# Kernel optimization log

Measured on AMD Instinct MI355X. Metric: run time of the kernel, lower is better.

Reference implementation:

```python
import jax, jax.numpy as jnp
import numpy as np

D_MODEL = 1024
N_HEADS = 16
HEAD_DIM = D_MODEL // N_HEADS
SPARSITY = 0.5  # torch.rand(...) < sparsity_factor -> True means masked (disallowed)


def setup_inputs() -> dict:
    key = jax.random.key(0)
    ks = jax.random.split(key, 12)
    B, S, D = 2, 2048, D_MODEL
    query = jax.random.normal(ks[0], (B, S, D), dtype=jnp.float32)
    key_t = jax.random.normal(ks[1], (B, S, D), dtype=jnp.float32)
    value = jax.random.normal(ks[2], (B, S, D), dtype=jnp.float32)
    # per-forward random boolean mask, materialized deterministically here
    mask = jax.random.uniform(ks[3], (B, S, S)) < SPARSITY
    scale = 1.0 / np.sqrt(D)
    Wq = jax.random.uniform(ks[4], (D, D), jnp.float32, -scale, scale)
    Wk = jax.random.uniform(ks[5], (D, D), jnp.float32, -scale, scale)
    Wv = jax.random.uniform(ks[6], (D, D), jnp.float32, -scale, scale)
    Wo = jax.random.uniform(ks[7], (D, D), jnp.float32, -scale, scale)
    bq = jnp.zeros((D,), jnp.float32)
    bk = jnp.zeros((D,), jnp.float32)
    bv = jnp.zeros((D,), jnp.float32)
    bo = jnp.zeros((D,), jnp.float32)
    return {"query": query, "key": key_t, "value": value, "mask": mask,
            "Wq": Wq, "Wk": Wk, "Wv": Wv, "Wo": Wo,
            "bq": bq, "bk": bk, "bv": bv, "bo": bo}


def reference(query, key, value, mask, Wq, Wk, Wv, Wo, bq, bk, bv, bo):
    B, S, D = query.shape
    H, hd = N_HEADS, HEAD_DIM
    # in-projections (torch uses x @ W.T + b)
    q = (query @ Wq.T + bq).reshape(B, S, H, hd).transpose(0, 2, 1, 3)  # (B,H,S,hd)
    k = (key @ Wk.T + bk).reshape(B, S, H, hd).transpose(0, 2, 1, 3)
    v = (value @ Wv.T + bv).reshape(B, S, H, hd).transpose(0, 2, 1, 3)
    scores = jnp.einsum('bhqd,bhkd->bhqk', q, k) / jnp.sqrt(jnp.float32(hd))
    # bool mask: True = disallowed; broadcast over heads
    scores = jnp.where(mask[:, None, :, :], -jnp.inf, scores)
    attn = jax.nn.softmax(scores, axis=-1)  # dropout inactive at eval
    out = jnp.einsum('bhqk,bhkd->bhqd', attn, v)  # (B,H,S,hd)
    out = out.transpose(0, 2, 1, 3).reshape(B, S, D)
    return out @ Wo.T + bo
```

## Files before the change

### kernel.cpp

```cpp
#include <hip/hip_runtime.h>
#include <stdint.h>

#define MTOK   4096
#define DMODEL 1024
#define SEQ    2048
#define NH     16
#define HD     64
#define LDK    72
#define QSCL   0.18033688f
#define NWORDS (2 * SEQ * SEQ / 64)

typedef _Float16 h8  __attribute__((ext_vector_type(8)));
typedef _Float16 h4  __attribute__((ext_vector_type(4)));
typedef _Float16 h2  __attribute__((ext_vector_type(2)));
typedef __fp16   fp16x2 __attribute__((ext_vector_type(2)));
typedef float    f16v __attribute__((ext_vector_type(16)));
typedef float    f4  __attribute__((ext_vector_type(4)));
typedef int      iv4 __attribute__((ext_vector_type(4)));

typedef __attribute__((address_space(1))) const unsigned int g_u32;
typedef __attribute__((address_space(3))) unsigned int       l_u32;

__device__ __forceinline__ void g2l16(const void* g, void* l) {
    __builtin_amdgcn_global_load_lds((g_u32*)(unsigned long long)g,
                                     (l_u32*)(unsigned int)(unsigned long long)l,
                                     16, 0, 0);
}

__device__ __forceinline__ h2 pkrtz(float a, float b) {
    fp16x2 r = __builtin_amdgcn_cvt_pkrtz(a, b);
    return __builtin_bit_cast(h2, r);
}

#if __has_builtin(__builtin_amdgcn_exp2f)
#define E2(x) __builtin_amdgcn_exp2f(x)
#else
#define E2(x) exp2f(x)
#endif

__device__ __forceinline__ float dot2sum(int v, float acc) {
    h2 a = __builtin_bit_cast(h2, v);
#if __has_builtin(__builtin_amdgcn_fdot2)
    h2 one2 = {(_Float16)1.0f, (_Float16)1.0f};
    return __builtin_amdgcn_fdot2(a, one2, acc, false);
#else
    return acc + (float)a.x + (float)a.y;
#endif
}

__global__ __launch_bounds__(256) void prep_kernel(
    const float* __restrict__ s0, const float* __restrict__ s1,
    const float* __restrict__ s2, const float* __restrict__ s3,
    const float* __restrict__ s4, const float* __restrict__ s5,
    const float* __restrict__ s6,
    _Float16* __restrict__ d0, _Float16* __restrict__ d1,
    _Float16* __restrict__ d2, _Float16* __restrict__ d3,
    _Float16* __restrict__ d4, _Float16* __restrict__ d5,
    _Float16* __restrict__ d6,
    const unsigned char* __restrict__ mb, const unsigned int* __restrict__ mu,
    unsigned long long* __restrict__ mout) {
    const int z = blockIdx.y;
    const int gid = blockIdx.x * 256 + threadIdx.x;
    const int stride = gridDim.x * 256;
    if (z < 7) {
        const float* s = (z == 0) ? s0 : (z == 1) ? s1 : (z == 2) ? s2
                       : (z == 3) ? s3 : (z == 4) ? s4 : (z == 5) ? s5 : s6;
        _Float16* d = (z == 0) ? d0 : (z == 1) ? d1 : (z == 2) ? d2
                    : (z == 3) ? d3 : (z == 4) ? d4 : (z == 5) ? d5 : d6;
        const int n4 = (z < 3) ? (MTOK * DMODEL / 4) : (DMODEL * DMODEL / 4);
        for (int i = gid; i < n4; i += stride) {
            float4 v = ((const float4*)s)[i];
            h4 o = {(_Float16)v.x, (_Float16)v.y, (_Float16)v.z, (_Float16)v.w};
            ((h4*)d)[i] = o;
        }
    } else {
        __shared__ int wsum[4];
        int cnt = 0;
        const uchar4* mp4 = (const uchar4*)mb;
#pragma unroll
        for (int i = 0; i < 8; ++i) {
            uchar4 v = mp4[threadIdx.x * 8 + i];
            cnt += (v.x != 0) + (v.y != 0) + (v.z != 0) + (v.w != 0);
        }
#pragma unroll
        for (int off = 32; off > 0; off >>= 1) cnt += __shfl_down(cnt, off, 64);
        if ((threadIdx.x & 63) == 0) wsum[threadIdx.x >> 6] = cnt;
        __syncthreads();
        const int byteflag = (wsum[0] + wsum[1] + wsum[2] + wsum[3]) > 2500;

        for (int w = gid; w < NWORDS; w += stride) {
            unsigned long long bits = 0ull;
            if (byteflag) {
                const uint4* p = (const uint4*)(mb + (size_t)w * 64);
#pragma unroll
                for (int i = 0; i < 4; ++i) {
                    uint4 v = p[i];
                    unsigned dw[4] = {v.x, v.y, v.z, v.w};
#pragma unroll
                    for (int j = 0; j < 4; ++j) {
                        unsigned d = dw[j];
                        unsigned nib = (unsigned)((d & 0xFFu) != 0)
                                     | ((unsigned)((d & 0xFF00u) != 0) << 1)
                                     | ((unsigned)((d & 0xFF0000u) != 0) << 2)
                                     | ((unsigned)((d >> 24) != 0) << 3);
                        bits |= (unsigned long long)nib << (i * 16 + j * 4);
                    }
                }
            } else {
                const uint4* p = (const uint4*)(mu + (size_t)w * 64);
#pragma unroll
                for (int i = 0; i < 16; ++i) {
                    uint4 v = p[i];
                    unsigned nib = (unsigned)(v.x != 0u)
                                 | ((unsigned)(v.y != 0u) << 1)
                                 | ((unsigned)(v.z != 0u) << 2)
                                 | ((unsigned)(v.w != 0u) << 3);
                    bits |= (unsigned long long)nib << (i * 4);
                }
            }
            mout[w] = bits;
        }
    }
}

template <int MODE, int BM, int BN>
__device__ __forceinline__ void gemm16_body(const _Float16* __restrict__ A,
                                            const _Float16* __restrict__ W,
                                            const float* __restrict__ bias,
                                            void* __restrict__ outv,
                                            float scale) {
    __shared__ __align__(16) _Float16 Asb[BM * 64];
    __shared__ __align__(16) _Float16 Bsb[BN * 64];
    constexpr int NI = BM / 32, NJ = BN / 32;
    constexpr int WM = BM / 2,  WN = BN / 2;
    constexpr int RA = BM * 128 / 4096;
    constexpr int RB = BN * 128 / 4096;
    const int tid = threadIdx.x;
    const int wv = tid >> 6, lane = tid & 63;
    const int l15 = lane & 15, g = lane >> 4;
    const int wy = wv >> 1, wx = wv & 1;
    const int m0 = blockIdx.x * BM, n0 = blockIdx.y * BN;

    f4 acc[NI][NJ];
#pragma unroll
    for (int i = 0; i < NI; ++i)
#pragma unroll
        for (int j = 0; j < NJ; ++j) acc[i][j] = (f4){0.f, 0.f, 0.f, 0.f};

    const char* Ab = (const char*)A;
    const char* Wb = (const char*)W;
    int srowA[RA], scolA[RA];
#pragma unroll
    for (int r = 0; r < RA; ++r) {
        const int o = (r * 256 + tid) * 16;
        srowA[r] = o >> 7;
        scolA[r] = (((o >> 4) & 7) ^ (srowA[r] & 7)) * 16;
    }
    int srowB[RB], scolB[RB];
#pragma unroll
    for (int r = 0; r < RB; ++r) {
        const int o = (r * 256 + tid) * 16;
        srowB[r] = o >> 7;
        scolB[r] = (((o >> 4) & 7) ^ (srowB[r] & 7)) * 16;
    }

    for (int kt = 0; kt < 16; ++kt) {
        const int k0b = kt * 128;
        __syncthreads();
#pragma unroll
        for (int r = 0; r < RA; ++r)
            g2l16(Ab + (size_t)(m0 + srowA[r]) * 2048 + k0b + scolA[r],
                  (char*)Asb + (r * 256 + tid) * 16);
#pragma unroll
        for (int r = 0; r < RB; ++r)
            g2l16(Wb + (size_t)(n0 + srowB[r]) * 2048 + k0b + scolB[r],
                  (char*)Bsb + (r * 256 + tid) * 16);
        __syncthreads();

#pragma unroll
        for (int ksub = 0; ksub < 2; ++ksub) {
            h8 af[NI], bf[NJ];
#pragma unroll
            for (int t = 0; t < NI; ++t) {
                const int row = wy * WM + t * 16 + l15;
                const int pos = (ksub * 4 + g) ^ (row & 7);
                af[t] = *(const h8*)(Asb + row * 64 + pos * 8);
            }
#pragma unroll
            for (int t = 0; t < NJ; ++t) {
                const int row = wx * WN + t * 16 + l15;
                const int pos = (ksub * 4 + g) ^ (row & 7);
                bf[t] = *(const h8*)(Bsb + row * 64 + pos * 8);
            }
#pragma unroll
            for (int i = 0; i < NI; ++i)
#pragma unroll
                for (int j = 0; j < NJ; ++j) {
                    if (MODE == 2)
                        acc[i][j] = __builtin_amdgcn_mfma_f32_16x16x32_f16(
                            bf[j], af[i], acc[i][j], 0, 0, 0);
                    else
                        acc[i][j] = __builtin_amdgcn_mfma_f32_16x16x32_f16(
                            af[i], bf[j], acc[i][j], 0, 0, 0);
                }
        }
    }

#pragma unroll
    for (int j = 0; j < NJ; ++j) {
#pragma unroll
        for (int i = 0; i < NI; ++i) {
            if (MODE == 2) {
                const int m = m0 + wy * WM + i * 16 + l15;
                const int b = m >> 11, s = m & 2047;
#pragma unroll
                for (int r = 0; r < 4; ++r) {
                    const int n = n0 + wx * WN + j * 16 + g * 4 + r;
                    const int h = n >> 6, d = n & 63;
                    ((_Float16*)outv)[(((size_t)(b * NH + h)) * HD + d) * SEQ + s] =
                        (_Float16)(acc[i][j][r] + bias[n]);
                }
            } else {
                const int n = n0 + wx * WN + j * 16 + l15;
                const float bb = bias[n];
                const int mbase = m0 + wy * WM + i * 16 + g * 4;
                if (MODE == 1) {
                    const int h = n >> 6, d = n & 63;
#pragma unroll
                    for (int r = 0; r < 4; ++r) {
                        const int m = mbase + r;
                        const int b = m >> 11, s = m & 2047;
                        ((_Float16*)outv)[(((size_t)(b * NH + h)) * SEQ + s) * HD + d] =
                            (_Float16)((acc[i][j][r] + bb) * scale);
                    }
                } else {
#pragma unroll
                    for (int r = 0; r < 4; ++r)
                        ((float*)outv)[(size_t)(mbase + r) * DMODEL + n] =
                            acc[i][j][r] + bb;
                }
            }
        }
    }
}

__global__ __launch_bounds__(256) void qkv_gemm16_kernel(
    const _Float16* __restrict__ xq, const _Float16* __restrict__ xk,
    const _Float16* __restrict__ xv,
    const _Float16* __restrict__ Wq, const _Float16* __restrict__ Wk,
    const _Float16* __restrict__ Wv,
    const float* __restrict__ bq, const float* __restrict__ bk,
    const float* __restrict__ bv,
    _Float16* __restrict__ q_out, _Float16* __restrict__ k_out,
    _Float16* __restrict__ vt_out) {
    const int z = blockIdx.z;
    if (z == 0)      gemm16_body<1, 128, 128>(xq, Wq, bq, (void*)q_out, QSCL);
    else if (z == 1) gemm16_body<1, 128, 128>(xk, Wk, bk, (void*)k_out, 1.0f);
    else             gemm16_body<2, 128, 128>(xv, Wv, bv, (void*)vt_out, 1.0f);
}

__global__ __launch_bounds__(256) void out_gemm16_kernel(
    const _Float16* __restrict__ X, const _Float16* __restrict__ W,
    const float* __restrict__ bias, float* __restrict__ out) {
    gemm16_body<0, 64, 128>(X, W, bias, (void*)out, 1.0f);
}

__global__ __launch_bounds__(512, 4) void attn_kernel(
    const _Float16* __restrict__ Q, const _Float16* __restrict__ K,
    const _Float16* __restrict__ Vt,
    const unsigned long long* __restrict__ mbits,
    _Float16* __restrict__ out) {
    __shared__ __align__(16) _Float16 Ks[2][2][64 * LDK];
    __shared__ __align__(16) _Float16 Vs[2][2][64 * LDK];

    const int tid = threadIdx.x;
    const int wv = tid >> 6, lane = tid & 63;
    const int grp = wv >> 2, wvg = wv & 3;
    const int l31 = lane & 31, hi = lane >> 5;
    const int q0 = blockIdx.x * 128;
    const int bh = blockIdx.y;
    const int b = bh >> 4, h = bh & 15;
    const size_t bho = (size_t)bh * (SEQ * HD);
    const int qrow = q0 + wvg * 32 + l31;

    h8 qf[4];
    const _Float16* qp = Q + bho + (size_t)qrow * HD;
#pragma unroll
    for (int ks = 0; ks < 4; ++ks) qf[ks] = *(const h8*)(qp + ks * 16 + hi * 8);

    f16v Ot[2];
#pragma unroll
    for (int mt = 0; mt < 2; ++mt)
#pragma unroll
        for (int r = 0; r < 16; ++r) Ot[mt][r] = 0.f;
    float l_r = 0.f;

    const int gtid = tid & 255;
    const int sr = gtid >> 2;
    const int scol = (gtid & 3) * 16;
    const _Float16* kg = K + bho;
    const _Float16* vg = Vt + bho;
    const unsigned long long* mrow =
        mbits + ((size_t)b * SEQ + qrow) * (SEQ / 64);

    {
        const int k0 = grp * 64;
        h8 a0 = *(const h8*)(kg + (size_t)(k0 + sr) * HD + scol);
        h8 a1 = *(const h8*)(kg + (size_t)(k0 + sr) * HD + scol + 8);
        h8 a2 = *(const h8*)(vg + (size_t)sr * SEQ + k0 + scol);
        h8 a3 = *(const h8*)(vg + (size_t)sr * SEQ + k0 + scol + 8);
        *(h8*)(&Ks[grp][0][sr * LDK + scol])     = a0;
        *(h8*)(&Ks[grp][0][sr * LDK + scol + 8]) = a1;
        *(h8*)(&Vs[grp][0][sr * LDK + scol])     = a2;
        *(h8*)(&Vs[grp][0][sr * LDK + scol + 8]) = a3;
    }
    uint2 mw = *(const uint2*)(mrow + grp);
    __syncthreads();

    for (int it = 0; it < 16; ++it) {
        const int cur = it & 1;
        const int kt = 2 * it + grp;
        h8 kr0, kr1, vr0, vr1;
        uint2 mw_n;
        if (it < 15) {
            const int k0n = (kt + 2) * 64;
            kr0 = *(const h8*)(kg + (size_t)(k0n + sr) * HD + scol);
            kr1 = *(const h8*)(kg + (size_t)(k0n + sr) * HD + scol + 8);
            vr0 = *(const h8*)(vg + (size_t)sr * SEQ + k0n + scol);
            vr1 = *(const h8*)(vg + (size_t)sr * SEQ + k0n + scol + 8);
            mw_n = *(const uint2*)(mrow + kt + 2);
        }

        f16v sc0, sc1;
#pragma unroll
        for (int r = 0; r < 16; ++r) { sc0[r] = 0.f; sc1[r] = 0.f; }
        __builtin_amdgcn_s_setprio(1);
#pragma unroll
        for (int ks = 0; ks < 4; ++ks) {
            h8 kf0 = *(const h8*)(&Ks[grp][cur][l31 * LDK + ks * 16 + hi * 8]);
            h8 kf1 = *(const h8*)(&Ks[grp][cur][(32 + l31) * LDK + ks * 16 + hi * 8]);
            sc0 = __builtin_amdgcn_mfma_f32_32x32x16_f16(kf0, qf[ks], sc0, 0, 0, 0);
            sc1 = __builtin_amdgcn_mfma_f32_32x32x16_f16(kf1, qf[ks], sc1, 0, 0, 0);
        }
        __builtin_amdgcn_s_setprio(0);

        int rp[8][2];
#pragma unroll
        for (int mt = 0; mt < 2; ++mt) {
            const unsigned w = mt ? mw.y : mw.x;
            const unsigned wl = w >> (hi * 4);
            const f16v& s = mt ? sc1 : sc0;
#pragma unroll
            for (int g4 = 0; g4 < 4; ++g4) {
                float p0 = E2(((wl >> (g4 * 8 + 0)) & 1u) ? -1e30f : s[g4 * 4 + 0]);
                float p1 = E2(((wl >> (g4 * 8 + 1)) & 1u) ? -1e30f : s[g4 * 4 + 1]);
                float p2 = E2(((wl >> (g4 * 8 + 2)) & 1u) ? -1e30f : s[g4 * 4 + 2]);
                float p3 = E2(((wl >> (g4 * 8 + 3)) & 1u) ? -1e30f : s[g4 * 4 + 3]);
                rp[mt * 4 + g4][0] = __builtin_bit_cast(int, pkrtz(p0, p1));
                rp[mt * 4 + g4][1] = __builtin_bit_cast(int, pkrtz(p2, p3));
            }
        }

        float l0 = 0.f, l1 = 0.f;
#pragma unroll
        for (int ks = 0; ks < 4; ++ks) {
            int a0 = rp[2 * ks][0], a1 = rp[2 * ks][1];
            int b0 = rp[2 * ks + 1][0], b1 = rp[2 * ks + 1][1];
            asm volatile("v_permlane32_swap_b32 %0, %1" : "+v"(a0), "+v"(b0));
            asm volatile("v_permlane32_swap_b32 %0, %1" : "+v"(a1), "+v"(b1));
            l0 = dot2sum(a0, l0); l1 = dot2sum(a1, l1);
            l0 = dot2sum(b0, l0); l1 = dot2sum(b1, l1);
            iv4 pi = {a0, a1, b0, b1};
            h8 pf = __builtin_bit_cast(h8, pi);
            __builtin_amdgcn_s_setprio(1);
            h8 vf0 = *(const h8*)(&Vs[grp][cur][l31 * LDK + ks * 16 + hi * 8]);
            h8 vf1 = *(const h8*)(&Vs[grp][cur][(32 + l31) * LDK + ks * 16 + hi * 8]);
            Ot[0] = __builtin_amdgcn_mfma_f32_32x32x16_f16(vf0, pf, Ot[0], 0, 0, 0);
            Ot[1] = __builtin_amdgcn_mfma_f32_32x32x16_f16(vf1, pf, Ot[1], 0, 0, 0);
            __builtin_amdgcn_s_setprio(0);
        }
        l_r += l0 + l1;

        if (it < 15) {
            const int nxt = cur ^ 1;
            *(h8*)(&Ks[grp][nxt][sr * LDK + scol])     = kr0;
            *(h8*)(&Ks[grp][nxt][sr * LDK + scol + 8]) = kr1;
            *(h8*)(&Vs[grp][nxt][sr * LDK + scol])     = vr0;
            *(h8*)(&Vs[grp][nxt][sr * LDK + scol + 8]) = vr1;
            mw = mw_n;
        }
        __syncthreads();
    }

    l_r += __shfl_xor(l_r, 32);
    float* mrg = (float*)&Ks[0][0][0];
    float* lm  = (float*)&Vs[0][0][0];
    const int ql = wvg * 32 + l31;
    if (grp == 1) {
#pragma unroll
        for (int mt = 0; mt < 2; ++mt)
#pragma unroll
            for (int t = 0; t < 4; ++t) {
                f4 v = {Ot[mt][t * 4 + 0], Ot[mt][t * 4 + 1],
                        Ot[mt][t * 4 + 2], Ot[mt][t * 4 + 3]};
                *(f4*)&mrg[ql * 64 + mt * 32 + t * 8 + hi * 4] = v;
            }
        if (hi == 0) lm[ql] = l_r;
    }
    __syncthreads();
    if (grp == 0) {
        l_r += lm[ql];
        const float inv = 1.0f / l_r;
        _Float16* op = out + ((size_t)b * SEQ + qrow) * DMODEL + h * HD;
#pragma unroll
        for (int mt = 0; mt < 2; ++mt)
#pragma unroll
            for (int t = 0; t < 4; ++t) {
                const int d = mt * 32 + t * 8 + hi * 4;
                f4 v = *(const f4*)&mrg[ql * 64 + d];
                h4 ov = {(_Float16)((Ot[mt][t * 4 + 0] + v.x) * inv),
                         (_Float16)((Ot[mt][t * 4 + 1] + v.y) * inv),
                         (_Float16)((Ot[mt][t * 4 + 2] + v.z) * inv),
                         (_Float16)((Ot[mt][t * 4 + 3] + v.w) * inv)};
                *(h4*)(op + d) = ov;
            }
    }
}

extern "C" void kernel_launch(void* const* d_in, const int* in_sizes, int n_in,
                              void* d_out, int out_size, void* d_ws, size_t ws_size,
                              hipStream_t stream) {
    const float* query = (const float*)d_in[0];
    const float* key_  = (const float*)d_in[1];
    const float* value = (const float*)d_in[2];
    const void*  mask  = d_in[3];
    const float* Wq = (const float*)d_in[4];
    const float* Wk = (const float*)d_in[5];
    const float* Wv = (const float*)d_in[6];
    const float* Wo = (const float*)d_in[7];
    const float* bq = (const float*)d_in[8];
    const float* bk = (const float*)d_in[9];
    const float* bv = (const float*)d_in[10];
    const float* bo = (const float*)d_in[11];

    char* ws = (char*)d_ws;
    _Float16* xq  = (_Float16*)(ws + 256);
    _Float16* xk  = xq + (size_t)MTOK * DMODEL;
    _Float16* xv  = xk + (size_t)MTOK * DMODEL;
    _Float16* Wqh = xv + (size_t)MTOK * DMODEL;
    _Float16* Wkh = Wqh + (size_t)DMODEL * DMODEL;
    _Float16* Wvh = Wkh + (size_t)DMODEL * DMODEL;
    _Float16* Woh = Wvh + (size_t)DMODEL * DMODEL;
    _Float16* q_ws  = Woh + (size_t)DMODEL * DMODEL;
    _Float16* k_ws  = q_ws + (size_t)MTOK * DMODEL;
    _Float16* vt_ws = k_ws + (size_t)MTOK * DMODEL;
    _Float16* a_ws  = vt_ws + (size_t)MTOK * DMODEL;
    unsigned long long* mb_ws =
        (unsigned long long*)(a_ws + (size_t)MTOK * DMODEL);

    prep_kernel<<<dim3(1024, 8), 256, 0, stream>>>(
        query, key_, value, Wq, Wk, Wv, Wo, xq, xk, xv, Wqh, Wkh, Wvh, Woh,
        (const unsigned char*)mask, (const unsigned int*)mask, mb_ws);

    dim3 gqkv(MTOK / 128, DMODEL / 128, 3);
    qkv_gemm16_kernel<<<gqkv, 256, 0, stream>>>(xq, xk, xv, Wqh, Wkh, Wvh,
                                                bq, bk, bv, q_ws, k_ws, vt_ws);

    dim3 gattn(SEQ / 128, 2 * NH);
    attn_kernel<<<gattn, 512, 0, stream>>>(q_ws, k_ws, vt_ws, mb_ws, a_ws);

    dim3 gout(MTOK / 64, DMODEL / 128);
    out_gemm16_kernel<<<gout, 256, 0, stream>>>(a_ws, Woh, bo, (float*)d_out);
}
```

Measured before the change: 269.6 us.

## Software-pipeline attention loop with async LDS loads and XOR-swizzled tiles

Replaces register-staged K/V copies with direct global-to-LDS loads (global_load_lds) and swaps the padded LDK layout for an XOR-swizzled 64-wide layout that avoids bank conflicts. The main loop is restructured so QK for tile t runs interleaved with softmax and PV of tile t-1, with prologue and epilogue stages. The aim is to hide load latency and overlap MFMA with exp work. It also cuts LDS footprint and register pressure from staging, but the async LDS writes depend on correct barriers, and the extra live score registers could pressure occupancy at 512 threads.

```diff
diff --git a/kernel.cpp b/kernel.cpp
--- a/kernel.cpp
+++ b/kernel.cpp
@@ -6,7 +6,6 @@
 #define SEQ    2048
 #define NH     16
 #define HD     64
-#define LDK    72
 #define QSCL   0.18033688f
 #define NWORDS (2 * SEQ * SEQ / 64)
 
@@ -270,8 +269,8 @@
     const _Float16* __restrict__ Vt,
     const unsigned long long* __restrict__ mbits,
     _Float16* __restrict__ out) {
-    __shared__ __align__(16) _Float16 Ks[2][2][64 * LDK];
-    __shared__ __align__(16) _Float16 Vs[2][2][64 * LDK];
+    __shared__ __align__(16) _Float16 Ks[2][2][4096];
+    __shared__ __align__(16) _Float16 Vs[2][2][4096];
 
     const int tid = threadIdx.x;
     const int wv = tid >> 6, lane = tid & 63;
@@ -296,101 +295,121 @@
     float l_r = 0.f;
 
     const int gtid = tid & 255;
-    const int sr = gtid >> 2;
-    const int scol = (gtid & 3) * 16;
+    const int srow = gtid >> 3;
+    const int schk = ((gtid & 7) ^ (srow & 7)) * 8;
     const _Float16* kg = K + bho;
     const _Float16* vg = Vt + bho;
     const unsigned long long* mrow =
         mbits + ((size_t)b * SEQ + qrow) * (SEQ / 64);
 
+#define STAGE_K(t, buf) do {                                               \
+    const int k0_ = (t) * 64;                                              \
+    g2l16(kg + (size_t)(k0_ + srow) * HD + schk,                           \
+          (char*)&Ks[grp][buf][0] + gtid * 16);                            \
+    g2l16(kg + (size_t)(k0_ + 32 + srow) * HD + schk,                      \
+          (char*)&Ks[grp][buf][0] + 4096 + gtid * 16);                     \
+} while (0)
+#define STAGE_V(t, buf) do {                                               \
+    const int k0_ = (t) * 64;                                              \
+    g2l16(vg + (size_t)srow * SEQ + k0_ + schk,                            \
+          (char*)&Vs[grp][buf][0] + gtid * 16);                            \
+    g2l16(vg + (size_t)(32 + srow) * SEQ + k0_ + schk,                     \
+          (char*)&Vs[grp][buf][0] + 4096 + gtid * 16);                     \
+} while (0)
+
+    int rp[8][2];
+    const int posx = (l31 & 7);
+#define SM_HALF(s, w, j0) do {                                             \
+    const unsigned wl = (w) >> (hi * 4);                                   \
+    _Pragma("unroll")                                                      \
+    for (int g4 = 0; g4 < 4; ++g4) {                                       \
+        float p0 = E2(((wl >> (g4 * 8 + 0)) & 1u) ? -1e30f : (s)[g4 * 4 + 0]); \
+        float p1 = E2(((wl >> (g4 * 8 + 1)) & 1u) ? -1e30f : (s)[g4 * 4 + 1]); \
+        float p2 = E2(((wl >> (g4 * 8 + 2)) & 1u) ? -1e30f : (s)[g4 * 4 + 2]); \
+        float p3 = E2(((wl >> (g4 * 8 + 3)) & 1u) ? -1e30f : (s)[g4 * 4 + 3]); \
+        rp[(j0) + g4][0] = __builtin_bit_cast(int, pkrtz(p0, p1));         \
+        rp[(j0) + g4][1] = __builtin_bit_cast(int, pkrtz(p2, p3));         \
+    }                                                                      \
+} while (0)
+
+#define QK_HALF(sc, roff) do {                                             \
+    _Pragma("unroll")                                                      \
+    for (int r = 0; r < 16; ++r) (sc)[r] = 0.f;                            \
+    __builtin_amdgcn_s_setprio(1);                                         \
+    _Pragma("unroll")                                                      \
+    for (int ks = 0; ks < 4; ++ks) {                                       \
+        h8 kf = *(const h8*)(&Ks[grp][cur][((roff) + l31) * 64 +           \
+                                           ((2 * ks + hi) ^ posx) * 8]);   \
+        (sc) = __builtin_amdgcn_mfma_f32_32x32x16_f16(kf, qf[ks], (sc),    \
+                                                      0, 0, 0);            \
+    }                                                                      \
+    __builtin_amdgcn_s_setprio(0);                                         \
+} while (0)
+
+#define PV_TILE(vbuf) do {                                                 \
+    float l0 = 0.f, l1 = 0.f;                                              \
+    _Pragma("unroll")                                                      \
+    for (int ks = 0; ks < 4; ++ks) {                                       \
+        int a0 = rp[2 * ks][0], a1 = rp[2 * ks][1];                        \
+        int b0 = rp[2 * ks + 1][0], b1 = rp[2 * ks + 1][1];                \
+        asm volatile("v_permlane32_swap_b32 %0, %1" : "+v"(a0), "+v"(b0)); \
+        asm volatile("v_permlane32_swap_b32 %0, %1" : "+v"(a1), "+v"(b1)); \
+        l0 = dot2sum(a0, l0); l1 = dot2sum(a1, l1);                        \
+        l0 = dot2sum(b0, l0); l1 = dot2sum(b1, l1);                        \
+        iv4 pi = {a0, a1, b0, b1};                                         \
+        h8 pf = __builtin_bit_cast(h8, pi);                                \
+        const int po = ((2 * ks + hi) ^ posx) * 8;                         \
+        h8 vf0 = *(const h8*)(&Vs[grp][vbuf][l31 * 64 + po]);              \
+        h8 vf1 = *(const h8*)(&Vs[grp][vbuf][(32 + l31) * 64 + po]);       \
+        __builtin_amdgcn_s_setprio(1);                                     \
+        Ot[0] = __builtin_amdgcn_mfma_f32_32x32x16_f16(vf0, pf, Ot[0],     \
+                                                       0, 0, 0);           \
+        Ot[1] = __builtin_amdgcn_mfma_f32_32x32x16_f16(vf1, pf, Ot[1],     \
+                                                       0, 0, 0);           \
+        __builtin_amdgcn_s_setprio(0);                                     \
+    }                                                                      \
+    l_r += l0 + l1;                                                        \
+} while (0)
+
+    f16v sc0, sc1;
+    uint2 mw = *(const uint2*)(mrow + grp);
+
+    STAGE_K(grp, 0);
+    __syncthreads();
     {
-        const int k0 = grp * 64;
-        h8 a0 = *(const h8*)(kg + (size_t)(k0 + sr) * HD + scol);
-        h8 a1 = *(const h8*)(kg + (size_t)(k0 + sr) * HD + scol + 8);
-        h8 a2 = *(const h8*)(vg + (size_t)sr * SEQ + k0 + scol);
-        h8 a3 = *(const h8*)(vg + (size_t)sr * SEQ + k0 + scol + 8);
-        *(h8*)(&Ks[grp][0][sr * LDK + scol])     = a0;
-        *(h8*)(&Ks[grp][0][sr * LDK + scol + 8]) = a1;
-        *(h8*)(&Vs[grp][0][sr * LDK + scol])     = a2;
-        *(h8*)(&Vs[grp][0][sr * LDK + scol + 8]) = a3;
-    }
-    uint2 mw = *(const uint2*)(mrow + grp);
-    __syncthreads();
-
-    for (int it = 0; it < 16; ++it) {
+        const int cur = 0;
+        STAGE_K(grp + 2, 1);
+        STAGE_V(grp, 0);
+        QK_HALF(sc0, 0);
+        QK_HALF(sc1, 32);
+        __syncthreads();
+    }
+
+    for (int it = 1; it < 16; ++it) {
         const int cur = it & 1;
         const int kt = 2 * it + grp;
-        h8 kr0, kr1, vr0, vr1;
-        uint2 mw_n;
-        if (it < 15) {
-            const int k0n = (kt + 2) * 64;
-            kr0 = *(const h8*)(kg + (size_t)(k0n + sr) * HD + scol);
-            kr1 = *(const h8*)(kg + (size_t)(k0n + sr) * HD + scol + 8);
-            vr0 = *(const h8*)(vg + (size_t)sr * SEQ + k0n + scol);
-            vr1 = *(const h8*)(vg + (size_t)sr * SEQ + k0n + scol + 8);
-            mw_n = *(const uint2*)(mrow + kt + 2);
-        }
-
-        f16v sc0, sc1;
-#pragma unroll
-        for (int r = 0; r < 16; ++r) { sc0[r] = 0.f; sc1[r] = 0.f; }
-        __builtin_amdgcn_s_setprio(1);
-#pragma unroll
-        for (int ks = 0; ks < 4; ++ks) {
-            h8 kf0 = *(const h8*)(&Ks[grp][cur][l31 * LDK + ks * 16 + hi * 8]);
-            h8 kf1 = *(const h8*)(&Ks[grp][cur][(32 + l31) * LDK + ks * 16 + hi * 8]);
-            sc0 = __builtin_amdgcn_mfma_f32_32x32x16_f16(kf0, qf[ks], sc0, 0, 0, 0);
-            sc1 = __builtin_amdgcn_mfma_f32_32x32x16_f16(kf1, qf[ks], sc1, 0, 0, 0);
-        }
-        __builtin_amdgcn_s_setprio(0);
-
-        int rp[8][2];
-#pragma unroll
-        for (int mt = 0; mt < 2; ++mt) {
-            const unsigned w = mt ? mw.y : mw.x;
-            const unsigned wl = w >> (hi * 4);
-            const f16v& s = mt ? sc1 : sc0;
-#pragma unroll
-            for (int g4 = 0; g4 < 4; ++g4) {
-                float p0 = E2(((wl >> (g4 * 8 + 0)) & 1u) ? -1e30f : s[g4 * 4 + 0]);
-                float p1 = E2(((wl >> (g4 * 8 + 1)) & 1u) ? -1e30f : s[g4 * 4 + 1]);
-                float p2 = E2(((wl >> (g4 * 8 + 2)) & 1u) ? -1e30f : s[g4 * 4 + 2]);
-                float p3 = E2(((wl >> (g4 * 8 + 3)) & 1u) ? -1e30f : s[g4 * 4 + 3]);
-                rp[mt * 4 + g4][0] = __builtin_bit_cast(int, pkrtz(p0, p1));
-                rp[mt * 4 + g4][1] = __builtin_bit_cast(int, pkrtz(p2, p3));
-            }
-        }
-
-        float l0 = 0.f, l1 = 0.f;
-#pragma unroll
-        for (int ks = 0; ks < 4; ++ks) {
-            int a0 = rp[2 * ks][0], a1 = rp[2 * ks][1];
-            int b0 = rp[2 * ks + 1][0], b1 = rp[2 * ks + 1][1];
-            asm volatile("v_permlane32_swap_b32 %0, %1" : "+v"(a0), "+v"(b0));
-            asm volatile("v_permlane32_swap_b32 %0, %1" : "+v"(a1), "+v"(b1));
-            l0 = dot2sum(a0, l0); l1 = dot2sum(a1, l1);
-            l0 = dot2sum(b0, l0); l1 = dot2sum(b1, l1);
-            iv4 pi = {a0, a1, b0, b1};
-            h8 pf = __builtin_bit_cast(h8, pi);
-            __builtin_amdgcn_s_setprio(1);
-            h8 vf0 = *(const h8*)(&Vs[grp][cur][l31 * LDK + ks * 16 + hi * 8]);
-            h8 vf1 = *(const h8*)(&Vs[grp][cur][(32 + l31) * LDK + ks * 16 + hi * 8]);
-            Ot[0] = __builtin_amdgcn_mfma_f32_32x32x16_f16(vf0, pf, Ot[0], 0, 0, 0);
-            Ot[1] = __builtin_amdgcn_mfma_f32_32x32x16_f16(vf1, pf, Ot[1], 0, 0, 0);
-            __builtin_amdgcn_s_setprio(0);
-        }
-        l_r += l0 + l1;
-
-        if (it < 15) {
-            const int nxt = cur ^ 1;
-            *(h8*)(&Ks[grp][nxt][sr * LDK + scol])     = kr0;
-            *(h8*)(&Ks[grp][nxt][sr * LDK + scol + 8]) = kr1;
-            *(h8*)(&Vs[grp][nxt][sr * LDK + scol])     = vr0;
-            *(h8*)(&Vs[grp][nxt][sr * LDK + scol + 8]) = vr1;
-            mw = mw_n;
-        }
+        if (it < 15) STAGE_K(kt + 2, cur ^ 1);
+        STAGE_V(kt, cur);
+        const uint2 mw_use = mw;
+        mw = *(const uint2*)(mrow + kt);
+
+        SM_HALF(sc0, mw_use.x, 0);
+        QK_HALF(sc0, 0);
+        SM_HALF(sc1, mw_use.y, 4);
+        QK_HALF(sc1, 32);
+        PV_TILE(cur ^ 1);
         __syncthreads();
     }
+
+    SM_HALF(sc0, mw.x, 0);
+    SM_HALF(sc1, mw.y, 4);
+    PV_TILE(1);
+
+#undef STAGE_K
+#undef STAGE_V
+#undef SM_HALF
+#undef QK_HALF
+#undef PV_TILE
 
     l_r += __shfl_xor(l_r, 32);
     float* mrg = (float*)&Ks[0][0][0];
```

Measured after the change: 288.6 us. +7.0%, slower.

## Split attention key range across blocks and add a combine kernel

Applied to the files above, without the earlier changes.

The attention grid gains a third dimension that splits the 2048 keys into two halves. Each block processes 1024 keys in 32-key tiles, split across two wave groups, and writes unnormalised fp32 partial outputs and row sums to workspace. A new combine kernel adds the two halves, normalises, and writes the fp16 attention output. The goal is to double the number of blocks (512 to 1024) and shrink shared memory per block for better occupancy, at the cost of extra global traffic for the partials, an extra launch, and smaller MFMA tiles per iteration.

```diff
diff --git a/kernel.cpp b/kernel.cpp
--- a/kernel.cpp
+++ b/kernel.cpp
@@ -6,7 +6,9 @@
 #define SEQ    2048
 #define NH     16
 #define HD     64
-#define LDK    72
+#define KVB    32
+#define LDKH   72
+#define LDVH   40
 #define QSCL   0.18033688f
 #define NWORDS (2 * SEQ * SEQ / 64)
 
@@ -269,20 +271,23 @@
     const _Float16* __restrict__ Q, const _Float16* __restrict__ K,
     const _Float16* __restrict__ Vt,
     const unsigned long long* __restrict__ mbits,
-    _Float16* __restrict__ out) {
-    __shared__ __align__(16) _Float16 Ks[2][2][64 * LDK];
-    __shared__ __align__(16) _Float16 Vs[2][2][64 * LDK];
+    float* __restrict__ pO, float* __restrict__ pl) {
+    __shared__ __align__(16) _Float16 shm[19456];
 
     const int tid = threadIdx.x;
     const int wv = tid >> 6, lane = tid & 63;
-    const int grp = wv >> 2, wvg = wv & 3;
+    const int str = wv >> 2, wvg = wv & 3;
     const int l31 = lane & 31, hi = lane >> 5;
     const int q0 = blockIdx.x * 128;
     const int bh = blockIdx.y;
-    const int b = bh >> 4, h = bh & 15;
+    const int khalf = blockIdx.z;
+    const int b = bh >> 4;
     const size_t bho = (size_t)bh * (SEQ * HD);
     const int qrow = q0 + wvg * 32 + l31;
 
+#define KT(bu) (&shm[(str * 2 + (bu)) * 2304])
+#define VT(bu) (&shm[9216 + (str * 2 + (bu)) * 2560])
+
     h8 qf[4];
     const _Float16* qp = Q + bho + (size_t)qrow * HD;
 #pragma unroll
@@ -296,74 +301,61 @@
     float l_r = 0.f;
 
     const int gtid = tid & 255;
-    const int sr = gtid >> 2;
-    const int scol = (gtid & 3) * 16;
+    const int krow = gtid >> 3, kcol = (gtid & 7) * 8;
+    const int vrow = gtid >> 2, vcol = (gtid & 3) * 8;
     const _Float16* kg = K + bho;
     const _Float16* vg = Vt + bho;
-    const unsigned long long* mrow =
-        mbits + ((size_t)b * SEQ + qrow) * (SEQ / 64);
+    const unsigned int* mrow32 = (const unsigned int*)mbits
+        + ((size_t)b * SEQ + qrow) * (SEQ / 32) + khalf * 32;
+    const int kb = khalf * 1024;
 
     {
-        const int k0 = grp * 64;
-        h8 a0 = *(const h8*)(kg + (size_t)(k0 + sr) * HD + scol);
-        h8 a1 = *(const h8*)(kg + (size_t)(k0 + sr) * HD + scol + 8);
-        h8 a2 = *(const h8*)(vg + (size_t)sr * SEQ + k0 + scol);
-        h8 a3 = *(const h8*)(vg + (size_t)sr * SEQ + k0 + scol + 8);
-        *(h8*)(&Ks[grp][0][sr * LDK + scol])     = a0;
-        *(h8*)(&Ks[grp][0][sr * LDK + scol + 8]) = a1;
-        *(h8*)(&Vs[grp][0][sr * LDK + scol])     = a2;
-        *(h8*)(&Vs[grp][0][sr * LDK + scol + 8]) = a3;
-    }
-    uint2 mw = *(const uint2*)(mrow + grp);
+        const int k0 = kb + str * KVB;
+        h8 kr = *(const h8*)(kg + (size_t)(k0 + krow) * HD + kcol);
+        h8 vr = *(const h8*)(vg + (size_t)vrow * SEQ + k0 + vcol);
+        *(h8*)(KT(0) + krow * LDKH + kcol) = kr;
+        *(h8*)(VT(0) + vrow * LDVH + vcol) = vr;
+    }
+    unsigned int mw = mrow32[str];
     __syncthreads();
 
     for (int it = 0; it < 16; ++it) {
         const int cur = it & 1;
-        const int kt = 2 * it + grp;
-        h8 kr0, kr1, vr0, vr1;
-        uint2 mw_n;
+        h8 kr, vr;
+        unsigned int mwn;
         if (it < 15) {
-            const int k0n = (kt + 2) * 64;
-            kr0 = *(const h8*)(kg + (size_t)(k0n + sr) * HD + scol);
-            kr1 = *(const h8*)(kg + (size_t)(k0n + sr) * HD + scol + 8);
-            vr0 = *(const h8*)(vg + (size_t)sr * SEQ + k0n + scol);
-            vr1 = *(const h8*)(vg + (size_t)sr * SEQ + k0n + scol + 8);
-            mw_n = *(const uint2*)(mrow + kt + 2);
-        }
-
-        f16v sc0, sc1;
-#pragma unroll
-        for (int r = 0; r < 16; ++r) { sc0[r] = 0.f; sc1[r] = 0.f; }
+            const int k0n = kb + (str + 2 * (it + 1)) * KVB;
+            kr = *(const h8*)(kg + (size_t)(k0n + krow) * HD + kcol);
+            vr = *(const h8*)(vg + (size_t)vrow * SEQ + k0n + vcol);
+            mwn = mrow32[str + 2 * (it + 1)];
+        }
+
+        f16v sc;
+#pragma unroll
+        for (int r = 0; r < 16; ++r) sc[r] = 0.f;
         __builtin_amdgcn_s_setprio(1);
 #pragma unroll
         for (int ks = 0; ks < 4; ++ks) {
-            h8 kf0 = *(const h8*)(&Ks[grp][cur][l31 * LDK + ks * 16 + hi * 8]);
-            h8 kf1 = *(const h8*)(&Ks[grp][cur][(32 + l31) * LDK + ks * 16 + hi * 8]);
-            sc0 = __builtin_amdgcn_mfma_f32_32x32x16_f16(kf0, qf[ks], sc0, 0, 0, 0);
-            sc1 = __builtin_amdgcn_mfma_f32_32x32x16_f16(kf1, qf[ks], sc1, 0, 0, 0);
+            h8 kf = *(const h8*)(KT(cur) + l31 * LDKH + ks * 16 + hi * 8);
+            sc = __builtin_amdgcn_mfma_f32_32x32x16_f16(kf, qf[ks], sc, 0, 0, 0);
         }
         __builtin_amdgcn_s_setprio(0);
 
-        int rp[8][2];
-#pragma unroll
-        for (int mt = 0; mt < 2; ++mt) {
-            const unsigned w = mt ? mw.y : mw.x;
-            const unsigned wl = w >> (hi * 4);
-            const f16v& s = mt ? sc1 : sc0;
-#pragma unroll
-            for (int g4 = 0; g4 < 4; ++g4) {
-                float p0 = E2(((wl >> (g4 * 8 + 0)) & 1u) ? -1e30f : s[g4 * 4 + 0]);
-                float p1 = E2(((wl >> (g4 * 8 + 1)) & 1u) ? -1e30f : s[g4 * 4 + 1]);
-                float p2 = E2(((wl >> (g4 * 8 + 2)) & 1u) ? -1e30f : s[g4 * 4 + 2]);
-                float p3 = E2(((wl >> (g4 * 8 + 3)) & 1u) ? -1e30f : s[g4 * 4 + 3]);
-                rp[mt * 4 + g4][0] = __builtin_bit_cast(int, pkrtz(p0, p1));
-                rp[mt * 4 + g4][1] = __builtin_bit_cast(int, pkrtz(p2, p3));
-            }
+        int rp[4][2];
+        const unsigned int wl = mw >> (hi * 4);
+#pragma unroll
+        for (int g4 = 0; g4 < 4; ++g4) {
+            float p0 = E2(((wl >> (g4 * 8 + 0)) & 1u) ? -1e30f : sc[g4 * 4 + 0]);
+            float p1 = E2(((wl >> (g4 * 8 + 1)) & 1u) ? -1e30f : sc[g4 * 4 + 1]);
+            float p2 = E2(((wl >> (g4 * 8 + 2)) & 1u) ? -1e30f : sc[g4 * 4 + 2]);
+            float p3 = E2(((wl >> (g4 * 8 + 3)) & 1u) ? -1e30f : sc[g4 * 4 + 3]);
+            rp[g4][0] = __builtin_bit_cast(int, pkrtz(p0, p1));
+            rp[g4][1] = __builtin_bit_cast(int, pkrtz(p2, p3));
         }
 
         float l0 = 0.f, l1 = 0.f;
 #pragma unroll
-        for (int ks = 0; ks < 4; ++ks) {
+        for (int ks = 0; ks < 2; ++ks) {
             int a0 = rp[2 * ks][0], a1 = rp[2 * ks][1];
             int b0 = rp[2 * ks + 1][0], b1 = rp[2 * ks + 1][1];
             asm volatile("v_permlane32_swap_b32 %0, %1" : "+v"(a0), "+v"(b0));
@@ -372,9 +364,9 @@
             l0 = dot2sum(b0, l0); l1 = dot2sum(b1, l1);
             iv4 pi = {a0, a1, b0, b1};
             h8 pf = __builtin_bit_cast(h8, pi);
+            h8 vf0 = *(const h8*)(VT(cur) + l31 * LDVH + ks * 16 + hi * 8);
+            h8 vf1 = *(const h8*)(VT(cur) + (32 + l31) * LDVH + ks * 16 + hi * 8);
             __builtin_amdgcn_s_setprio(1);
-            h8 vf0 = *(const h8*)(&Vs[grp][cur][l31 * LDK + ks * 16 + hi * 8]);
-            h8 vf1 = *(const h8*)(&Vs[grp][cur][(32 + l31) * LDK + ks * 16 + hi * 8]);
             Ot[0] = __builtin_amdgcn_mfma_f32_32x32x16_f16(vf0, pf, Ot[0], 0, 0, 0);
             Ot[1] = __builtin_amdgcn_mfma_f32_32x32x16_f16(vf1, pf, Ot[1], 0, 0, 0);
             __builtin_amdgcn_s_setprio(0);
@@ -382,21 +374,18 @@
         l_r += l0 + l1;
 
         if (it < 15) {
-            const int nxt = cur ^ 1;
-            *(h8*)(&Ks[grp][nxt][sr * LDK + scol])     = kr0;
-            *(h8*)(&Ks[grp][nxt][sr * LDK + scol + 8]) = kr1;
-            *(h8*)(&Vs[grp][nxt][sr * LDK + scol])     = vr0;
-            *(h8*)(&Vs[grp][nxt][sr * LDK + scol + 8]) = vr1;
-            mw = mw_n;
+            *(h8*)(KT(cur ^ 1) + krow * LDKH + kcol) = kr;
+            *(h8*)(VT(cur ^ 1) + vrow * LDVH + vcol) = vr;
+            mw = mwn;
         }
         __syncthreads();
     }
 
     l_r += __shfl_xor(l_r, 32);
-    float* mrg = (float*)&Ks[0][0][0];
-    float* lm  = (float*)&Vs[0][0][0];
+    float* mrg = (float*)&shm[0];
+    float* lm  = (float*)&shm[0] + 8192;
     const int ql = wvg * 32 + l31;
-    if (grp == 1) {
+    if (str == 1) {
 #pragma unroll
         for (int mt = 0; mt < 2; ++mt)
 #pragma unroll
@@ -408,23 +397,47 @@
         if (hi == 0) lm[ql] = l_r;
     }
     __syncthreads();
-    if (grp == 0) {
-        l_r += lm[ql];
-        const float inv = 1.0f / l_r;
-        _Float16* op = out + ((size_t)b * SEQ + qrow) * DMODEL + h * HD;
+    if (str == 0) {
 #pragma unroll
         for (int mt = 0; mt < 2; ++mt)
 #pragma unroll
             for (int t = 0; t < 4; ++t) {
-                const int d = mt * 32 + t * 8 + hi * 4;
-                f4 v = *(const f4*)&mrg[ql * 64 + d];
-                h4 ov = {(_Float16)((Ot[mt][t * 4 + 0] + v.x) * inv),
-                         (_Float16)((Ot[mt][t * 4 + 1] + v.y) * inv),
-                         (_Float16)((Ot[mt][t * 4 + 2] + v.z) * inv),
-                         (_Float16)((Ot[mt][t * 4 + 3] + v.w) * inv)};
-                *(h4*)(op + d) = ov;
-            }
-    }
+                f4* p = (f4*)&mrg[ql * 64 + mt * 32 + t * 8 + hi * 4];
+                f4 v = *p;
+                v[0] += Ot[mt][t * 4 + 0]; v[1] += Ot[mt][t * 4 + 1];
+                v[2] += Ot[mt][t * 4 + 2]; v[3] += Ot[mt][t * 4 + 3];
+                *p = v;
+            }
+        if (hi == 0) lm[ql] += l_r;
+    }
+    __syncthreads();
+    float* po = pO + ((size_t)(khalf * 32 + bh) * SEQ + q0) * 64;
+    const f4* ms = (const f4*)mrg;
+#pragma unroll
+    for (int r = 0; r < 4; ++r) {
+        const int i4 = r * 512 + tid;
+        ((f4*)po)[i4] = ms[i4];
+    }
+    if (tid < 128) pl[(size_t)(khalf * 32 + bh) * SEQ + q0 + tid] = lm[tid];
+#undef KT
+#undef VT
+}
+
+__global__ __launch_bounds__(256) void combine_kernel(
+    const float* __restrict__ pO, const float* __restrict__ pl,
+    _Float16* __restrict__ out) {
+    const int gid = blockIdx.x * 256 + threadIdx.x;
+    const int dq = gid & 15;
+    const int s  = (gid >> 4) & 2047;
+    const int bh = gid >> 15;
+    const f4 o0 = ((const f4*)pO)[((size_t)bh * SEQ + s) * 16 + dq];
+    const f4 o1 = ((const f4*)pO)[((size_t)(32 + bh) * SEQ + s) * 16 + dq];
+    const float inv = 1.0f /
+        (pl[(size_t)bh * SEQ + s] + pl[(size_t)(32 + bh) * SEQ + s]);
+    const int b = bh >> 4, h = bh & 15;
+    h4 r = {(_Float16)((o0[0] + o1[0]) * inv), (_Float16)((o0[1] + o1[1]) * inv),
+            (_Float16)((o0[2] + o1[2]) * inv), (_Float16)((o0[3] + o1[3]) * inv)};
+    *(h4*)(out + (((size_t)(b * SEQ + s)) * NH + h) * HD + dq * 4) = r;
 }
 
 extern "C" void kernel_launch(void* const* d_in, const int* in_sizes, int n_in,
@@ -444,19 +457,21 @@
     const float* bo = (const float*)d_in[11];
 
     char* ws = (char*)d_ws;
-    _Float16* xq  = (_Float16*)(ws + 256);
-    _Float16* xk  = xq + (size_t)MTOK * DMODEL;
-    _Float16* xv  = xk + (size_t)MTOK * DMODEL;
-    _Float16* Wqh = xv + (size_t)MTOK * DMODEL;
-    _Float16* Wkh = Wqh + (size_t)DMODEL * DMODEL;
-    _Float16* Wvh = Wkh + (size_t)DMODEL * DMODEL;
-    _Float16* Woh = Wvh + (size_t)DMODEL * DMODEL;
+    _Float16* Woh  = (_Float16*)(ws + 256);
     _Float16* q_ws  = Woh + (size_t)DMODEL * DMODEL;
     _Float16* k_ws  = q_ws + (size_t)MTOK * DMODEL;
     _Float16* vt_ws = k_ws + (size_t)MTOK * DMODEL;
     _Float16* a_ws  = vt_ws + (size_t)MTOK * DMODEL;
     unsigned long long* mb_ws =
         (unsigned long long*)(a_ws + (size_t)MTOK * DMODEL);
+    _Float16* xq  = (_Float16*)((char*)mb_ws + (1 << 20));
+    _Float16* xk  = xq + (size_t)MTOK * DMODEL;
+    _Float16* xv  = xk + (size_t)MTOK * DMODEL;
+    _Float16* Wqh = xv + (size_t)MTOK * DMODEL;
+    _Float16* Wkh = Wqh + (size_t)DMODEL * DMODEL;
+    _Float16* Wvh = Wkh + (size_t)DMODEL * DMODEL;
+    float* pO = (float*)xq;
+    float* pl = (float*)((char*)xq + (32u << 20));
 
     prep_kernel<<<dim3(1024, 8), 256, 0, stream>>>(
         query, key_, value, Wq, Wk, Wv, Wo, xq, xk, xv, Wqh, Wkh, Wvh, Woh,
@@ -466,8 +481,11 @@
     qkv_gemm16_kernel<<<gqkv, 256, 0, stream>>>(xq, xk, xv, Wqh, Wkh, Wvh,
                                                 bq, bk, bv, q_ws, k_ws, vt_ws);
 
-    dim3 gattn(SEQ / 128, 2 * NH);
-    attn_kernel<<<gattn, 512, 0, stream>>>(q_ws, k_ws, vt_ws, mb_ws, a_ws);
+    dim3 gattn(SEQ / 128, 2 * NH, 2);
+    attn_kernel<<<gattn, 512, 0, stream>>>(q_ws, k_ws, vt_ws, mb_ws, pO, pl);
+
+    combine_kernel<<<dim3(2 * NH * SEQ * (HD / 4) / 256), 256, 0, stream>>>(
+        pO, pl, a_ws);
 
     dim3 gout(MTOK / 64, DMODEL / 128);
     out_gemm16_kernel<<<gout, 256, 0, stream>>>(a_ws, Woh, bo, (float*)d_out);
```

After: 289.7 us. 7.4% more time.

## Stage K/V tiles via direct global-to-LDS loads with XOR swizzle and mask LUT

Applied to the files above, without the earlier changes.

Replaces register-staged K/V prefetch (global load into VGPRs then LDS store) with global_load_lds direct copies into an XOR-swizzled unpadded LDS layout. This removes the staging registers and the LDS write instructions, and avoids bank conflicts through the swizzle instead of padding. Masking is also changed: a 16-entry LUT in LDS turns each 4-bit mask nibble into fp16 AND masks applied after exp, instead of per-element selects. The merge buffer stride is padded to 68. The risk is that the async LDS loads need correct wait/sync ordering, and the kernel now relies on __syncthreads to cover them.

```diff
diff --git a/kernel.cpp b/kernel.cpp
--- a/kernel.cpp
+++ b/kernel.cpp
@@ -6,7 +6,7 @@
 #define SEQ    2048
 #define NH     16
 #define HD     64
-#define LDK    72
+#define LDP    68
 #define QSCL   0.18033688f
 #define NWORDS (2 * SEQ * SEQ / 64)
 
@@ -270,8 +270,7 @@
     const _Float16* __restrict__ Vt,
     const unsigned long long* __restrict__ mbits,
     _Float16* __restrict__ out) {
-    __shared__ __align__(16) _Float16 Ks[2][2][64 * LDK];
-    __shared__ __align__(16) _Float16 Vs[2][2][64 * LDK];
+    __shared__ __align__(16) _Float16 shm[32768 + 64];
 
     const int tid = threadIdx.x;
     const int wv = tid >> 6, lane = tid & 63;
@@ -283,6 +282,12 @@
     const size_t bho = (size_t)bh * (SEQ * HD);
     const int qrow = q0 + wvg * 32 + l31;
 
+    if (tid < 16) {
+        unsigned mlo = (tid & 1 ? 0u : 0xFFFFu) | (tid & 2 ? 0u : 0xFFFF0000u);
+        unsigned mhi = (tid & 4 ? 0u : 0xFFFFu) | (tid & 8 ? 0u : 0xFFFF0000u);
+        ((uint2*)&shm[32768])[tid] = (uint2){mlo, mhi};
+    }
+
     h8 qf[4];
     const _Float16* qp = Q + bho + (size_t)qrow * HD;
 #pragma unroll
@@ -296,40 +301,44 @@
     float l_r = 0.f;
 
     const int gtid = tid & 255;
-    const int sr = gtid >> 2;
-    const int scol = (gtid & 3) * 16;
+    const int srow = gtid >> 3;
+    const int schk = ((gtid & 7) ^ (srow & 7)) * 8;
     const _Float16* kg = K + bho;
     const _Float16* vg = Vt + bho;
     const unsigned long long* mrow =
         mbits + ((size_t)b * SEQ + qrow) * (SEQ / 64);
 
-    {
-        const int k0 = grp * 64;
-        h8 a0 = *(const h8*)(kg + (size_t)(k0 + sr) * HD + scol);
-        h8 a1 = *(const h8*)(kg + (size_t)(k0 + sr) * HD + scol + 8);
-        h8 a2 = *(const h8*)(vg + (size_t)sr * SEQ + k0 + scol);
-        h8 a3 = *(const h8*)(vg + (size_t)sr * SEQ + k0 + scol + 8);
-        *(h8*)(&Ks[grp][0][sr * LDK + scol])     = a0;
-        *(h8*)(&Ks[grp][0][sr * LDK + scol + 8]) = a1;
-        *(h8*)(&Vs[grp][0][sr * LDK + scol])     = a2;
-        *(h8*)(&Vs[grp][0][sr * LDK + scol + 8]) = a3;
-    }
+    _Float16* KTb = &shm[grp * 2 * 4096];
+    _Float16* VTb = &shm[16384 + grp * 2 * 4096];
+    const int px = l31 & 7;
+
+#define STAGE(t, buf) do {                                                  \
+    const int k0_ = (t) * 64;                                               \
+    char* kd = (char*)(KTb + (buf) * 4096);                                 \
+    char* vd = (char*)(VTb + (buf) * 4096);                                 \
+    g2l16(kg + (size_t)(k0_ + srow) * HD + schk,       kd + gtid * 16);     \
+    g2l16(kg + (size_t)(k0_ + 32 + srow) * HD + schk,  kd + 4096 + gtid * 16); \
+    g2l16(vg + (size_t)srow * SEQ + k0_ + schk,        vd + gtid * 16);     \
+    g2l16(vg + (size_t)(32 + srow) * SEQ + k0_ + schk, vd + 4096 + gtid * 16); \
+} while (0)
+
     uint2 mw = *(const uint2*)(mrow + grp);
+    STAGE(grp, 0);
     __syncthreads();
+
+    const uint2* lut = (const uint2*)&shm[32768];
+    int rp[8][2];
 
     for (int it = 0; it < 16; ++it) {
         const int cur = it & 1;
         const int kt = 2 * it + grp;
-        h8 kr0, kr1, vr0, vr1;
-        uint2 mw_n;
+        uint2 mwn;
         if (it < 15) {
-            const int k0n = (kt + 2) * 64;
-            kr0 = *(const h8*)(kg + (size_t)(k0n + sr) * HD + scol);
-            kr1 = *(const h8*)(kg + (size_t)(k0n + sr) * HD + scol + 8);
-            vr0 = *(const h8*)(vg + (size_t)sr * SEQ + k0n + scol);
-            vr1 = *(const h8*)(vg + (size_t)sr * SEQ + k0n + scol + 8);
-            mw_n = *(const uint2*)(mrow + kt + 2);
-        }
+            STAGE(kt + 2, cur ^ 1);
+            mwn = *(const uint2*)(mrow + kt + 2);
+        }
+        const _Float16* Kc = KTb + cur * 4096;
+        const _Float16* Vc = VTb + cur * 4096;
 
         f16v sc0, sc1;
 #pragma unroll
@@ -337,14 +346,14 @@
         __builtin_amdgcn_s_setprio(1);
 #pragma unroll
         for (int ks = 0; ks < 4; ++ks) {
-            h8 kf0 = *(const h8*)(&Ks[grp][cur][l31 * LDK + ks * 16 + hi * 8]);
-            h8 kf1 = *(const h8*)(&Ks[grp][cur][(32 + l31) * LDK + ks * 16 + hi * 8]);
+            const int po = ((2 * ks + hi) ^ px) * 8;
+            h8 kf0 = *(const h8*)(Kc + l31 * 64 + po);
+            h8 kf1 = *(const h8*)(Kc + (32 + l31) * 64 + po);
             sc0 = __builtin_amdgcn_mfma_f32_32x32x16_f16(kf0, qf[ks], sc0, 0, 0, 0);
             sc1 = __builtin_amdgcn_mfma_f32_32x32x16_f16(kf1, qf[ks], sc1, 0, 0, 0);
         }
         __builtin_amdgcn_s_setprio(0);
 
-        int rp[8][2];
 #pragma unroll
         for (int mt = 0; mt < 2; ++mt) {
             const unsigned w = mt ? mw.y : mw.x;
@@ -352,12 +361,15 @@
             const f16v& s = mt ? sc1 : sc0;
 #pragma unroll
             for (int g4 = 0; g4 < 4; ++g4) {
-                float p0 = E2(((wl >> (g4 * 8 + 0)) & 1u) ? -1e30f : s[g4 * 4 + 0]);
-                float p1 = E2(((wl >> (g4 * 8 + 1)) & 1u) ? -1e30f : s[g4 * 4 + 1]);
-                float p2 = E2(((wl >> (g4 * 8 + 2)) & 1u) ? -1e30f : s[g4 * 4 + 2]);
-                float p3 = E2(((wl >> (g4 * 8 + 3)) & 1u) ? -1e30f : s[g4 * 4 + 3]);
-                rp[mt * 4 + g4][0] = __builtin_bit_cast(int, pkrtz(p0, p1));
-                rp[mt * 4 + g4][1] = __builtin_bit_cast(int, pkrtz(p2, p3));
+                const uint2 m2 = lut[(wl >> (g4 * 8)) & 15u];
+                float p0 = E2(s[g4 * 4 + 0]);
+                float p1 = E2(s[g4 * 4 + 1]);
+                float p2 = E2(s[g4 * 4 + 2]);
+                float p3 = E2(s[g4 * 4 + 3]);
+                rp[mt * 4 + g4][0] =
+                    __builtin_bit_cast(int, pkrtz(p0, p1)) & (int)m2.x;
+                rp[mt * 4 + g4][1] =
+                    __builtin_bit_cast(int, pkrtz(p2, p3)) & (int)m2.y;
             }
         }
 
@@ -372,29 +384,24 @@
             l0 = dot2sum(b0, l0); l1 = dot2sum(b1, l1);
             iv4 pi = {a0, a1, b0, b1};
             h8 pf = __builtin_bit_cast(h8, pi);
+            const int po = ((2 * ks + hi) ^ px) * 8;
+            h8 vf0 = *(const h8*)(Vc + l31 * 64 + po);
+            h8 vf1 = *(const h8*)(Vc + (32 + l31) * 64 + po);
             __builtin_amdgcn_s_setprio(1);
-            h8 vf0 = *(const h8*)(&Vs[grp][cur][l31 * LDK + ks * 16 + hi * 8]);
-            h8 vf1 = *(const h8*)(&Vs[grp][cur][(32 + l31) * LDK + ks * 16 + hi * 8]);
             Ot[0] = __builtin_amdgcn_mfma_f32_32x32x16_f16(vf0, pf, Ot[0], 0, 0, 0);
             Ot[1] = __builtin_amdgcn_mfma_f32_32x32x16_f16(vf1, pf, Ot[1], 0, 0, 0);
             __builtin_amdgcn_s_setprio(0);
         }
         l_r += l0 + l1;
 
-        if (it < 15) {
-            const int nxt = cur ^ 1;
-            *(h8*)(&Ks[grp][nxt][sr * LDK + scol])     = kr0;
-            *(h8*)(&Ks[grp][nxt][sr * LDK + scol + 8]) = kr1;
-            *(h8*)(&Vs[grp][nxt][sr * LDK + scol])     = vr0;
-            *(h8*)(&Vs[grp][nxt][sr * LDK + scol + 8]) = vr1;
-            mw = mw_n;
-        }
+        if (it < 15) mw = mwn;
         __syncthreads();
     }
+#undef STAGE
 
     l_r += __shfl_xor(l_r, 32);
-    float* mrg = (float*)&Ks[0][0][0];
-    float* lm  = (float*)&Vs[0][0][0];
+    float* mrg = (float*)&shm[0];
+    float* lm  = mrg + 128 * LDP;
     const int ql = wvg * 32 + l31;
     if (grp == 1) {
 #pragma unroll
@@ -403,7 +410,7 @@
             for (int t = 0; t < 4; ++t) {
                 f4 v = {Ot[mt][t * 4 + 0], Ot[mt][t * 4 + 1],
                         Ot[mt][t * 4 + 2], Ot[mt][t * 4 + 3]};
-                *(f4*)&mrg[ql * 64 + mt * 32 + t * 8 + hi * 4] = v;
+                *(f4*)&mrg[ql * LDP + mt * 32 + t * 8 + hi * 4] = v;
             }
         if (hi == 0) lm[ql] = l_r;
     }
@@ -417,7 +424,7 @@
 #pragma unroll
             for (int t = 0; t < 4; ++t) {
                 const int d = mt * 32 + t * 8 + hi * 4;
-                f4 v = *(const f4*)&mrg[ql * 64 + d];
+                f4 v = *(const f4*)&mrg[ql * LDP + d];
                 h4 ov = {(_Float16)((Ot[mt][t * 4 + 0] + v.x) * inv),
                          (_Float16)((Ot[mt][t * 4 + 1] + v.y) * inv),
                          (_Float16)((Ot[mt][t * 4 + 2] + v.z) * inv),
```

Result: no change. 268.1 us (-0.6%).
